# Performance work log

Measured on AMD Instinct MI355X. Metric: run time of the kernel, lower is better.

Reference implementation:

```python
import jax, jax.numpy as jnp
import numpy as np

B = 512          # graphs
M = 200          # nodes per graph
N = B * M        # 102400 total nodes
E = N * 32       # 3,276,800 edges
DIM_IN = 128
K = 30           # SortPool k
F = 32 + 32 + 32 + 1  # concat feature dim = 97


def setup_inputs() -> dict:
    key = jax.random.key(0)
    ks = jax.random.split(key, 20)
    x = jax.random.normal(ks[0], (N, DIM_IN), jnp.float32)
    # within-graph random edges so that batched SortPool is meaningful
    eg = jnp.repeat(jnp.arange(B, dtype=jnp.int32), E // B)  # graph id per edge
    src = eg * M + jax.random.randint(ks[1], (E,), 0, M, dtype=jnp.int32)
    dst = eg * M + jax.random.randint(ks[2], (E,), 0, M, dtype=jnp.int32)
    edge_index = jnp.stack([src, dst])  # [2, E]
    batch = jnp.arange(N, dtype=jnp.int32) // M  # sorted graph assignment

    def lin(k, fi, fo):
        s = 1.0 / np.sqrt(fi)
        return jax.random.uniform(k, (fi, fo), jnp.float32, -s, s)

    inp = {
        "x": x, "edge_index": edge_index, "batch": batch,
        "W1": lin(ks[3], DIM_IN, 32), "b1": jnp.zeros((32,), jnp.float32),
        "W2": lin(ks[4], 32, 32), "b2": jnp.zeros((32,), jnp.float32),
        "W3": lin(ks[5], 32, 32), "b3": jnp.zeros((32,), jnp.float32),
        "W4": lin(ks[6], 32, 1),  "b4": jnp.zeros((1,), jnp.float32),
        "convW1": jax.random.normal(ks[7], (16, 1, 97), jnp.float32) * 0.05,
        "convb1": jnp.zeros((16,), jnp.float32),
        "convW2": jax.random.normal(ks[8], (32, 16, 5), jnp.float32) * 0.05,
        "convb2": jnp.zeros((32,), jnp.float32),
        "linW1": lin(ks[9], 352, 128), "linb1": jnp.zeros((128,), jnp.float32),
        "linW2": lin(ks[10], 128, 1),  "linb2": jnp.zeros((1,), jnp.float32),
    }
    return inp


def _gcn(x, W, b, src, dst, dinv):
    """PyG GCNConv: D^-1/2 (A+I) D^-1/2 X W + b (degrees include self-loops)."""
    xw = x @ W                                   # [N, Fout]
    norm = dinv[src] * dinv[dst]                 # [E]
    agg = jax.ops.segment_sum(xw[src] * norm[:, None], dst, num_segments=N)
    agg = agg + xw * (dinv * dinv)[:, None]      # self-loop term
    return agg + b


def reference(x, edge_index, batch, W1, b1, W2, b2, W3, b3, W4, b4,
              convW1, convb1, convW2, convb2, linW1, linb1, linW2, linb2):
    src, dst = edge_index[0], edge_index[1]
    deg = jax.ops.segment_sum(jnp.ones((E,), x.dtype), dst, num_segments=N) + 1.0
    dinv = jax.lax.rsqrt(deg)

    h1 = jnp.tanh(_gcn(x, W1, b1, src, dst, dinv))
    h2 = jnp.tanh(_gcn(h1, W2, b2, src, dst, dinv))
    h3 = jnp.tanh(_gcn(h2, W3, b3, src, dst, dinv))
    h4 = jnp.tanh(_gcn(h3, W4, b4, src, dst, dinv))
    h = jnp.concatenate([h1, h2, h3, h4], axis=-1)  # [N, 97]

    # SortPool: batch is block-contiguous with M nodes/graph -> dense [B, M, F]
    hd = h.reshape(B, M, F)
    order = jnp.argsort(-hd[:, :, -1], axis=1)[:, :K]          # top-K by last channel
    top = jnp.take_along_axis(hd, order[:, :, None], axis=1)   # [B, K, 97]

    seq = top.reshape(B, 1, K * F)                             # [B, 1, 2910]
    dn = ("NCH", "OIH", "NCH")
    c1 = jax.lax.conv_general_dilated(seq, convW1, (97,), "VALID",
                                      dimension_numbers=dn) + convb1[None, :, None]
    c1 = jax.nn.relu(c1)                                       # [B, 16, 30]
    c1 = c1.reshape(B, 16, 15, 2).max(axis=-1)                 # MaxPool1d(2,2)
    c2 = jax.lax.conv_general_dilated(c1, convW2, (1,), "VALID",
                                      dimension_numbers=dn) + convb2[None, :, None]
    c2 = jax.nn.relu(c2)                                       # [B, 32, 11]

    flat = c2.reshape(B, 352)
    hlin = jax.nn.relu(flat @ linW1 + linb1)                   # dropout = identity (eval)
    out = jax.nn.sigmoid(hlin @ linW2 + linb2)                 # [B, 1]
    return out
```

## Files before the change

### kernel.cpp

```cpp
#include <hip/hip_runtime.h>
#include <hip/hip_fp16.h>


#define TPB   1024
#define GRID  512
#define MG    200
#define EPG   6400
#define EE    (512 * EPG)

#define OFF_BUFX 0
#define OFF_HCUR 28944
#define OFF_CSR  57744
#define OFF_ROFF 64944
#define OFF_CNT  65760
#define OFF_CUR  66560
#define OFF_DINV 67360
#define OFF_H4   68160
#define OFF_RANK 68960
#define OFF_ORD  69760
#define OFF_BIAS 69880
#define OFF_RED  70072
#define OFF_WREG 70144
#define SMEM_BYTES 78336

__global__ __launch_bounds__(TPB)
void dgcnn_kernel(
    const float* __restrict__ x,
    const int*   __restrict__ ei,
    const float* __restrict__ W1, const float* __restrict__ b1,
    const float* __restrict__ W2, const float* __restrict__ b2,
    const float* __restrict__ W3, const float* __restrict__ b3,
    const float* __restrict__ W4, const float* __restrict__ b4,
    const float* __restrict__ cW1, const float* __restrict__ cb1,
    const float* __restrict__ cW2, const float* __restrict__ cb2,
    const float* __restrict__ lW1, const float* __restrict__ lb1,
    const float* __restrict__ lW2, const float* __restrict__ lb2,
    __half* __restrict__ arch,
    float* __restrict__ out)
{
    extern __shared__ unsigned char smem[];
    float* bufX = (float*)(smem + OFF_BUFX);
    float* hcur = (float*)(smem + OFF_HCUR);
    unsigned char* csr = (unsigned char*)(smem + OFF_CSR);
    int*   roff = (int*)(smem + OFF_ROFF);
    int*   cnt  = (int*)(smem + OFF_CNT);
    int*   cur  = (int*)(smem + OFF_CUR);
    float* dinv = (float*)(smem + OFF_DINV);
    float* h4k  = (float*)(smem + OFF_H4);
    int*   rank = (int*)(smem + OFF_RANK);
    int*   ord  = (int*)(smem + OFF_ORD);
    float* bias = (float*)(smem + OFF_BIAS);
    float* red  = (float*)(smem + OFF_RED);
    float* wreg = (float*)(smem + OFF_WREG);

    const int g = blockIdx.x;
    const int t = threadIdx.x;
    const int gbase = g * MG;
    const float* xg   = x + (size_t)gbase * 128;
    const int*   srcp = ei + (size_t)g * EPG;
    const int*   dstp = ei + (size_t)EE + (size_t)g * EPG;

    for (int idx = t; idx < 2048; idx += TPB) wreg[idx] = W1[idx];
    if (t < 32) bias[t] = b1[t];
    if (t < MG) { cnt[t] = 0; rank[t] = 0; }
    if (t >= 512 && t < 548) bufX[200 * 36 + (t - 512)] = 0.f;
    __syncthreads();

    for (int e = t; e < EPG; e += TPB) atomicAdd(&cnt[dstp[e] - gbase], 1);
    __syncthreads();

    if (t >= 256 && t < 256 + MG) {
        int i = t - 256;
        dinv[i] = 1.0f / sqrtf((float)(cnt[i] + 1));
    }
    if (t < 64) {
        if (t == 0) roff[0] = 0;
        int carry = 0;
        #pragma unroll
        for (int c = 0; c < 4; ++c) {
            const int i = c * 64 + t;
            int v = (i < MG) ? ((cnt[i] + 4) & ~3) : 0;
            #pragma unroll
            for (int off = 1; off < 64; off <<= 1) {
                int u = __shfl_up(v, off);
                if (t >= (int)off) v += u;
            }
            if (i < MG) roff[i + 1] = carry + v;
            carry += __shfl(v, 63);
        }
    }
    __syncthreads();

    if (t < MG) {
        int p = roff[t];
        csr[p] = (unsigned char)t;
        cur[t] = p + 1;
    }
    __syncthreads();

    for (int e = t; e < EPG; e += TPB) {
        int d = dstp[e] - gbase;
        int s = srcp[e] - gbase;
        int p = atomicAdd(&cur[d], 1);
        csr[p] = (unsigned char)s;
    }
    __syncthreads();

    if (t < MG) {
        for (int p = cur[t]; p < roff[t + 1]; ++p) csr[p] = (unsigned char)200;
    }
    __syncthreads();

    const int f32lane = t & 31;
    const int islot   = t >> 5;

    auto agg_layer = [&](int archOff) {
        const int fq  = t & 7;
        const int f4  = fq << 2;
        const int dsl = t >> 3;
        for (int d = dsl; d < MG; d += 128) {
            const int p0 = roff[d], p1 = roff[d + 1];
            float a0 = 0.f, a1 = 0.f, a2 = 0.f, a3 = 0.f;
            for (int p = p0; p < p1; p += 4) {
                const unsigned q = *(const unsigned*)(csr + p);
                const float4 v0 = *(const float4*)(bufX + (q & 255u) * 36 + f4);
                const float4 v1 = *(const float4*)(bufX + ((q >> 8) & 255u) * 36 + f4);
                a0 += v0.x; a1 += v0.y; a2 += v0.z; a3 += v0.w;
                a0 += v1.x; a1 += v1.y; a2 += v1.z; a3 += v1.w;
                const float4 v2 = *(const float4*)(bufX + ((q >> 16) & 255u) * 36 + f4);
                const float4 v3 = *(const float4*)(bufX + (q >> 24) * 36 + f4);
                a0 += v2.x; a1 += v2.y; a2 += v2.z; a3 += v2.w;
                a0 += v3.x; a1 += v3.y; a2 += v3.z; a3 += v3.w;
            }
            const float dv = dinv[d];
            const float o0 = tanhf(dv * a0 + bias[f4 + 0]);
            const float o1 = tanhf(dv * a1 + bias[f4 + 1]);
            const float o2 = tanhf(dv * a2 + bias[f4 + 2]);
            const float o3 = tanhf(dv * a3 + bias[f4 + 3]);
            *(float4*)(hcur + d * 36 + f4) = make_float4(o0, o1, o2, o3);
            if (archOff >= 0) {
                const __half2 p01 = __floats2half2_rn(o0, o1);
                const __half2 p23 = __floats2half2_rn(o2, o3);
                __half2* dst = (__half2*)(arch + (size_t)(gbase + d) * 64 + archOff + f4);
                dst[0] = p01;
                dst[1] = p23;
            }
        }
    };

    auto gemm_mid = [&](const float* __restrict__ src) {
        const int f = f32lane;
        {
            float acc0 = 0.f, acc1 = 0.f, acc2 = 0.f, acc3 = 0.f;
            #pragma unroll 2
            for (int k4 = 0; k4 < 8; ++k4) {
                const float w0 = wreg[k4 * 128 + 0  + f];
                const float w1 = wreg[k4 * 128 + 32 + f];
                const float w2 = wreg[k4 * 128 + 64 + f];
                const float w3 = wreg[k4 * 128 + 96 + f];
                float4 v;
                v = *(const float4*)(src + (islot      ) * 36 + k4 * 4); acc0 += v.x*w0 + v.y*w1 + v.z*w2 + v.w*w3;
                v = *(const float4*)(src + (islot + 32 ) * 36 + k4 * 4); acc1 += v.x*w0 + v.y*w1 + v.z*w2 + v.w*w3;
                v = *(const float4*)(src + (islot + 64 ) * 36 + k4 * 4); acc2 += v.x*w0 + v.y*w1 + v.z*w2 + v.w*w3;
                v = *(const float4*)(src + (islot + 96 ) * 36 + k4 * 4); acc3 += v.x*w0 + v.y*w1 + v.z*w2 + v.w*w3;
            }
            bufX[(islot      ) * 36 + f] = dinv[islot      ] * acc0;
            bufX[(islot + 32 ) * 36 + f] = dinv[islot + 32 ] * acc1;
            bufX[(islot + 64 ) * 36 + f] = dinv[islot + 64 ] * acc2;
            bufX[(islot + 96 ) * 36 + f] = dinv[islot + 96 ] * acc3;
        }
        {
            const int i2  = islot + 192;
            const int i2c = i2 < MG ? i2 : (MG - 1);
            float acc0 = 0.f, acc1 = 0.f, acc2 = 0.f;
            #pragma unroll 2
            for (int k4 = 0; k4 < 8; ++k4) {
                const float w0 = wreg[k4 * 128 + 0  + f];
                const float w1 = wreg[k4 * 128 + 32 + f];
                const float w2 = wreg[k4 * 128 + 64 + f];
                const float w3 = wreg[k4 * 128 + 96 + f];
                float4 v;
                v = *(const float4*)(src + (islot + 128) * 36 + k4 * 4); acc0 += v.x*w0 + v.y*w1 + v.z*w2 + v.w*w3;
                v = *(const float4*)(src + (islot + 160) * 36 + k4 * 4); acc1 += v.x*w0 + v.y*w1 + v.z*w2 + v.w*w3;
                v = *(const float4*)(src + (i2c        ) * 36 + k4 * 4); acc2 += v.x*w0 + v.y*w1 + v.z*w2 + v.w*w3;
            }
            bufX[(islot + 128) * 36 + f] = dinv[islot + 128] * acc0;
            bufX[(islot + 160) * 36 + f] = dinv[islot + 160] * acc1;
            if (i2 < MG) bufX[i2 * 36 + f] = dinv[i2] * acc2;
        }
    };

    {
        const int f = f32lane;
        const float4* xv = (const float4*)xg;
        float a0 = 0.f, a1 = 0.f, a2 = 0.f, a3 = 0.f;
        #pragma unroll 2
        for (int k4 = 0; k4 < 16; ++k4) {
            const float w0 = wreg[k4 * 128 + 0  + f];
            const float w1 = wreg[k4 * 128 + 32 + f];
            const float w2 = wreg[k4 * 128 + 64 + f];
            const float w3 = wreg[k4 * 128 + 96 + f];
            float4 v;
            v = xv[(islot      ) * 32 + k4]; a0 += v.x*w0 + v.y*w1 + v.z*w2 + v.w*w3;
            v = xv[(islot + 32 ) * 32 + k4]; a1 += v.x*w0 + v.y*w1 + v.z*w2 + v.w*w3;
            v = xv[(islot + 64 ) * 32 + k4]; a2 += v.x*w0 + v.y*w1 + v.z*w2 + v.w*w3;
            v = xv[(islot + 96 ) * 32 + k4]; a3 += v.x*w0 + v.y*w1 + v.z*w2 + v.w*w3;
        }
        __syncthreads();
        for (int idx = t; idx < 2048; idx += TPB) wreg[idx] = W1[2048 + idx];
        __syncthreads();
        #pragma unroll 2
        for (int k4 = 0; k4 < 16; ++k4) {
            const float w0 = wreg[k4 * 128 + 0  + f];
            const float w1 = wreg[k4 * 128 + 32 + f];
            const float w2 = wreg[k4 * 128 + 64 + f];
            const float w3 = wreg[k4 * 128 + 96 + f];
            float4 v;
            v = xv[(islot      ) * 32 + 16 + k4]; a0 += v.x*w0 + v.y*w1 + v.z*w2 + v.w*w3;
            v = xv[(islot + 32 ) * 32 + 16 + k4]; a1 += v.x*w0 + v.y*w1 + v.z*w2 + v.w*w3;
            v = xv[(islot + 64 ) * 32 + 16 + k4]; a2 += v.x*w0 + v.y*w1 + v.z*w2 + v.w*w3;
            v = xv[(islot + 96 ) * 32 + 16 + k4]; a3 += v.x*w0 + v.y*w1 + v.z*w2 + v.w*w3;
        }
        bufX[(islot      ) * 36 + f] = dinv[islot      ] * a0;
        bufX[(islot + 32 ) * 36 + f] = dinv[islot + 32 ] * a1;
        bufX[(islot + 64 ) * 36 + f] = dinv[islot + 64 ] * a2;
        bufX[(islot + 96 ) * 36 + f] = dinv[islot + 96 ] * a3;
        const int r6  = islot + 192;
        const int r6c = (r6 < MG) ? r6 : (MG - 1);
        float b0v = 0.f, b1v = 0.f, b2v = 0.f;
        #pragma unroll 2
        for (int k4 = 0; k4 < 16; ++k4) {
            const float w0 = wreg[k4 * 128 + 0  + f];
            const float w1 = wreg[k4 * 128 + 32 + f];
            const float w2 = wreg[k4 * 128 + 64 + f];
            const float w3 = wreg[k4 * 128 + 96 + f];
            float4 v;
            v = xv[(islot + 128) * 32 + 16 + k4]; b0v += v.x*w0 + v.y*w1 + v.z*w2 + v.w*w3;
            v = xv[(islot + 160) * 32 + 16 + k4]; b1v += v.x*w0 + v.y*w1 + v.z*w2 + v.w*w3;
            v = xv[(r6c        ) * 32 + 16 + k4]; b2v += v.x*w0 + v.y*w1 + v.z*w2 + v.w*w3;
        }
        __syncthreads();
        for (int idx = t; idx < 2048; idx += TPB) wreg[idx] = W1[idx];
        __syncthreads();
        #pragma unroll 2
        for (int k4 = 0; k4 < 16; ++k4) {
            const float w0 = wreg[k4 * 128 + 0  + f];
            const float w1 = wreg[k4 * 128 + 32 + f];
            const float w2 = wreg[k4 * 128 + 64 + f];
            const float w3 = wreg[k4 * 128 + 96 + f];
            float4 v;
            v = xv[(islot + 128) * 32 + k4]; b0v += v.x*w0 + v.y*w1 + v.z*w2 + v.w*w3;
            v = xv[(islot + 160) * 32 + k4]; b1v += v.x*w0 + v.y*w1 + v.z*w2 + v.w*w3;
            v = xv[(r6c        ) * 32 + k4]; b2v += v.x*w0 + v.y*w1 + v.z*w2 + v.w*w3;
        }
        bufX[(islot + 128) * 36 + f] = dinv[islot + 128] * b0v;
        bufX[(islot + 160) * 36 + f] = dinv[islot + 160] * b1v;
        if (r6 < MG) bufX[r6 * 36 + f] = dinv[r6] * b2v;
    }
    __syncthreads();
    agg_layer(0);
    __syncthreads();

    for (int idx = t; idx < 1024; idx += TPB) wreg[idx] = W2[idx];
    if (t < 32) bias[t] = b2[t];
    __syncthreads();
    gemm_mid(hcur);
    __syncthreads();
    agg_layer(32);
    __syncthreads();

    for (int idx = t; idx < 1024; idx += TPB) wreg[idx] = W3[idx];
    if (t < 32) bias[t] = b3[t];
    __syncthreads();
    gemm_mid(hcur);
    __syncthreads();
    agg_layer(-1);
    __syncthreads();

    float* scl = (float*)(smem + OFF_CNT);
    if (t < MG) {
        float a = 0.f;
        #pragma unroll 8
        for (int k = 0; k < 32; ++k) a += hcur[t * 36 + k] * W4[k];
        scl[t] = dinv[t] * a;
    }
    if (t == 512) scl[200] = 0.f;
    __syncthreads();
    if (t < MG) {
        const int p0 = roff[t], p1 = roff[t + 1];
        float s = 0.f;
        for (int p = p0; p < p1; p += 4) {
            const unsigned q = *(const unsigned*)(csr + p);
            s += scl[q & 255u] + scl[(q >> 8) & 255u]
               + scl[(q >> 16) & 255u] + scl[q >> 24];
        }
        h4k[t] = tanhf(dinv[t] * s + b4[0]);
    }
    __syncthreads();

    if (t < 512) {
        const int i = t & 255;
        const int half = t >> 8;
        if (i < MG) {
            const float vi = h4k[i];
            int r = 0;
            const int j0 = half * 100, j1 = half * 100 + 100;
            for (int j = j0; j < j1; ++j) {
                const float vj = h4k[j];
                r += (vj > vi || (vj == vi && j < i)) ? 1 : 0;
            }
            atomicAdd(&rank[i], r);
        }
    }
    __syncthreads();
    if (t < MG) {
        const int r = rank[t];
        if (r < 30) ord[r] = t;
    }
    __syncthreads();

    float* topv = bufX;
    float* cw   = bufX + 3104;
    for (int idx = t; idx < 1552; idx += TPB) cw[idx] = cW1[idx];
    for (int idx = t; idx < 2560; idx += TPB) cw[1552 + idx] = cW2[idx];
    if (t < 16) bias[t] = cb1[t];
    else if (t < 48) bias[t] = cb2[t - 16];
    for (int idx = t; idx < 2910; idx += TPB) {
        const int kk = idx / 97;
        const int ff = idx - kk * 97;
        const int nd = ord[kk];
        float v;
        if      (ff < 64) v = __half2float(arch[(size_t)(gbase + nd) * 64 + ff]);
        else if (ff < 96) v = hcur[nd * 36 + (ff - 64)];
        else              v = h4k[nd];
        topv[kk * 100 + ff] = v;
    }
    __syncthreads();

    float* c1p2 = hcur;
    float* c1pl = hcur + 480;
    float* flat = hcur + 736;
    float* hlin = hcur + 1088;

    if (t < 480) {
        const int o  = t & 15;
        const int tt = t >> 4;
        float a = bias[o];
        const float* wrow = cw + o * 97;
        const float* trow = topv + tt * 100;
        #pragma unroll 4
        for (int f = 0; f < 97; ++f) a += wrow[f] * trow[f];
        c1p2[o * 30 + tt] = fmaxf(a, 0.f);
    }
    __syncthreads();

    if (t < 240) {
        const int o  = t & 15;
        const int tp = t >> 4;
        c1pl[o * 16 + tp] = fmaxf(c1p2[o * 30 + 2 * tp], c1p2[o * 30 + 2 * tp + 1]);
    }
    __syncthreads();

    if (t < 352) {
        const int o  = t & 31;
        const int tt = t >> 5;
        float a = bias[16 + o];
        const float* w2r = cw + 1552 + o * 80;
        #pragma unroll
        for (int i2 = 0; i2 < 16; ++i2) {
            #pragma unroll
            for (int kk = 0; kk < 5; ++kk)
                a += w2r[i2 * 5 + kk] * c1pl[i2 * 16 + tt + kk];
        }
        flat[o * 11 + tt] = fmaxf(a, 0.f);
    } else if (t >= 512 && t < 640) {
        hlin[t - 512] = lb1[t - 512];
    }
    __syncthreads();

    {
        const int f  = t & 127;
        const int kc = t >> 7;
        float a = 0.f;
        const int k0 = kc * 44;
        #pragma unroll 4
        for (int kk = k0; kk < k0 + 44; ++kk) a += flat[kk] * lW1[kk * 128 + f];
        atomicAdd(&hlin[f], a);
    }
    __syncthreads();

    if (t < 128) {
        float p = fmaxf(hlin[t], 0.f) * lW2[t];
        #pragma unroll
        for (int off = 32; off > 0; off >>= 1) p += __shfl_down(p, off);
        if ((t & 63) == 0) red[t >> 6] = p;
    }
    __syncthreads();
    if (t == 0) {
        const float z = red[0] + red[1] + lb2[0];
        out[g] = 1.f / (1.f + expf(-z));
    }
}

extern "C" void kernel_launch(void* const* d_in, const int* in_sizes, int n_in,
                              void* d_out, int out_size, void* d_ws, size_t ws_size,
                              hipStream_t stream) {
    (void)in_sizes; (void)n_in; (void)out_size; (void)ws_size;
    const float* x   = (const float*)d_in[0];
    const int*   ei  = (const int*)d_in[1];
    const float* W1  = (const float*)d_in[3];  const float* b1  = (const float*)d_in[4];
    const float* W2  = (const float*)d_in[5];  const float* b2  = (const float*)d_in[6];
    const float* W3  = (const float*)d_in[7];  const float* b3  = (const float*)d_in[8];
    const float* W4  = (const float*)d_in[9];  const float* b4  = (const float*)d_in[10];
    const float* cW1 = (const float*)d_in[11]; const float* cb1 = (const float*)d_in[12];
    const float* cW2 = (const float*)d_in[13]; const float* cb2 = (const float*)d_in[14];
    const float* lW1 = (const float*)d_in[15]; const float* lb1 = (const float*)d_in[16];
    const float* lW2 = (const float*)d_in[17]; const float* lb2 = (const float*)d_in[18];
    float* out = (float*)d_out;
    __half* arch = (__half*)d_ws;

    hipFuncSetAttribute((const void*)dgcnn_kernel,
                        hipFuncAttributeMaxDynamicSharedMemorySize, SMEM_BYTES);

    dgcnn_kernel<<<GRID, TPB, SMEM_BYTES, stream>>>(
        x, ei, W1, b1, W2, b2, W3, b3, W4, b4,
        cW1, cb1, cW2, cb2, lW1, lb1, lW2, lb2, arch, out);
}
```

Measured before the change: 281.4 us.

## Halve block size to 512 threads and read W1 directly from global memory

Block size drops from 1024 to 512 threads, and every per-thread loop (aggregation, GEMMs, final linear layer) is rewritten so each thread covers twice as many rows or columns. The first-layer GEMM no longer stages W1 through shared memory in two halves with extra barriers. It reads W1 straight from global memory or cache, which shrinks LDS use and lets more blocks fit per CU. In exchange each block has less parallelism, and the W1 reads are repeated global loads instead of LDS hits.

```diff
diff --git a/kernel.cpp b/kernel.cpp
--- a/kernel.cpp
+++ b/kernel.cpp
@@ -2,7 +2,7 @@
 #include <hip/hip_fp16.h>
 
 
-#define TPB   1024
+#define TPB   512
 #define GRID  512
 #define MG    200
 #define EPG   6400
@@ -21,7 +21,7 @@
 #define OFF_BIAS 69880
 #define OFF_RED  70072
 #define OFF_WREG 70144
-#define SMEM_BYTES 78336
+#define SMEM_BYTES 74240
 
 __global__ __launch_bounds__(TPB)
 void dgcnn_kernel(
@@ -60,10 +60,9 @@
     const int*   srcp = ei + (size_t)g * EPG;
     const int*   dstp = ei + (size_t)EE + (size_t)g * EPG;
 
-    for (int idx = t; idx < 2048; idx += TPB) wreg[idx] = W1[idx];
     if (t < 32) bias[t] = b1[t];
     if (t < MG) { cnt[t] = 0; rank[t] = 0; }
-    if (t >= 512 && t < 548) bufX[200 * 36 + (t - 512)] = 0.f;
+    if (t >= 256 && t < 292) bufX[200 * 36 + (t - 256)] = 0.f;
     __syncthreads();
 
     for (int e = t; e < EPG; e += TPB) atomicAdd(&cnt[dstp[e] - gbase], 1);
@@ -118,7 +117,7 @@
         const int fq  = t & 7;
         const int f4  = fq << 2;
         const int dsl = t >> 3;
-        for (int d = dsl; d < MG; d += 128) {
+        for (int d = dsl; d < MG; d += 64) {
             const int p0 = roff[d], p1 = roff[d + 1];
             float a0 = 0.f, a1 = 0.f, a2 = 0.f, a3 = 0.f;
             for (int p = p0; p < p1; p += 4) {
@@ -150,8 +149,10 @@
 
     auto gemm_mid = [&](const float* __restrict__ src) {
         const int f = f32lane;
-        {
-            float acc0 = 0.f, acc1 = 0.f, acc2 = 0.f, acc3 = 0.f;
+        #pragma unroll
+        for (int j0 = 0; j0 < 12; j0 += 4) {
+            const int r0 = islot + 16 * j0;
+            float a0 = 0.f, a1 = 0.f, a2 = 0.f, a3 = 0.f;
             #pragma unroll 2
             for (int k4 = 0; k4 < 8; ++k4) {
                 const float w0 = wreg[k4 * 128 + 0  + f];
@@ -159,103 +160,70 @@
                 const float w2 = wreg[k4 * 128 + 64 + f];
                 const float w3 = wreg[k4 * 128 + 96 + f];
                 float4 v;
-                v = *(const float4*)(src + (islot      ) * 36 + k4 * 4); acc0 += v.x*w0 + v.y*w1 + v.z*w2 + v.w*w3;
-                v = *(const float4*)(src + (islot + 32 ) * 36 + k4 * 4); acc1 += v.x*w0 + v.y*w1 + v.z*w2 + v.w*w3;
-                v = *(const float4*)(src + (islot + 64 ) * 36 + k4 * 4); acc2 += v.x*w0 + v.y*w1 + v.z*w2 + v.w*w3;
-                v = *(const float4*)(src + (islot + 96 ) * 36 + k4 * 4); acc3 += v.x*w0 + v.y*w1 + v.z*w2 + v.w*w3;
-            }
-            bufX[(islot      ) * 36 + f] = dinv[islot      ] * acc0;
-            bufX[(islot + 32 ) * 36 + f] = dinv[islot + 32 ] * acc1;
-            bufX[(islot + 64 ) * 36 + f] = dinv[islot + 64 ] * acc2;
-            bufX[(islot + 96 ) * 36 + f] = dinv[islot + 96 ] * acc3;
-        }
-        {
-            const int i2  = islot + 192;
-            const int i2c = i2 < MG ? i2 : (MG - 1);
-            float acc0 = 0.f, acc1 = 0.f, acc2 = 0.f;
+                v = *(const float4*)(src + (r0      ) * 36 + k4 * 4); a0 += v.x*w0 + v.y*w1 + v.z*w2 + v.w*w3;
+                v = *(const float4*)(src + (r0 + 16 ) * 36 + k4 * 4); a1 += v.x*w0 + v.y*w1 + v.z*w2 + v.w*w3;
+                v = *(const float4*)(src + (r0 + 32 ) * 36 + k4 * 4); a2 += v.x*w0 + v.y*w1 + v.z*w2 + v.w*w3;
+                v = *(const float4*)(src + (r0 + 48 ) * 36 + k4 * 4); a3 += v.x*w0 + v.y*w1 + v.z*w2 + v.w*w3;
+            }
+            bufX[(r0      ) * 36 + f] = dinv[r0      ] * a0;
+            bufX[(r0 + 16 ) * 36 + f] = dinv[r0 + 16 ] * a1;
+            bufX[(r0 + 32 ) * 36 + f] = dinv[r0 + 32 ] * a2;
+            bufX[(r0 + 48 ) * 36 + f] = dinv[r0 + 48 ] * a3;
+        }
+        if (islot < 8) {
+            const int r = 192 + islot;
+            float a0 = 0.f;
             #pragma unroll 2
             for (int k4 = 0; k4 < 8; ++k4) {
                 const float w0 = wreg[k4 * 128 + 0  + f];
                 const float w1 = wreg[k4 * 128 + 32 + f];
                 const float w2 = wreg[k4 * 128 + 64 + f];
                 const float w3 = wreg[k4 * 128 + 96 + f];
-                float4 v;
-                v = *(const float4*)(src + (islot + 128) * 36 + k4 * 4); acc0 += v.x*w0 + v.y*w1 + v.z*w2 + v.w*w3;
-                v = *(const float4*)(src + (islot + 160) * 36 + k4 * 4); acc1 += v.x*w0 + v.y*w1 + v.z*w2 + v.w*w3;
-                v = *(const float4*)(src + (i2c        ) * 36 + k4 * 4); acc2 += v.x*w0 + v.y*w1 + v.z*w2 + v.w*w3;
-            }
-            bufX[(islot + 128) * 36 + f] = dinv[islot + 128] * acc0;
-            bufX[(islot + 160) * 36 + f] = dinv[islot + 160] * acc1;
-            if (i2 < MG) bufX[i2 * 36 + f] = dinv[i2] * acc2;
+                const float4 v = *(const float4*)(src + r * 36 + k4 * 4);
+                a0 += v.x*w0 + v.y*w1 + v.z*w2 + v.w*w3;
+            }
+            bufX[r * 36 + f] = dinv[r] * a0;
         }
     };
 
     {
         const int f = f32lane;
         const float4* xv = (const float4*)xg;
-        float a0 = 0.f, a1 = 0.f, a2 = 0.f, a3 = 0.f;
-        #pragma unroll 2
-        for (int k4 = 0; k4 < 16; ++k4) {
-            const float w0 = wreg[k4 * 128 + 0  + f];
-            const float w1 = wreg[k4 * 128 + 32 + f];
-            const float w2 = wreg[k4 * 128 + 64 + f];
-            const float w3 = wreg[k4 * 128 + 96 + f];
-            float4 v;
-            v = xv[(islot      ) * 32 + k4]; a0 += v.x*w0 + v.y*w1 + v.z*w2 + v.w*w3;
-            v = xv[(islot + 32 ) * 32 + k4]; a1 += v.x*w0 + v.y*w1 + v.z*w2 + v.w*w3;
-            v = xv[(islot + 64 ) * 32 + k4]; a2 += v.x*w0 + v.y*w1 + v.z*w2 + v.w*w3;
-            v = xv[(islot + 96 ) * 32 + k4]; a3 += v.x*w0 + v.y*w1 + v.z*w2 + v.w*w3;
-        }
-        __syncthreads();
-        for (int idx = t; idx < 2048; idx += TPB) wreg[idx] = W1[2048 + idx];
-        __syncthreads();
-        #pragma unroll 2
-        for (int k4 = 0; k4 < 16; ++k4) {
-            const float w0 = wreg[k4 * 128 + 0  + f];
-            const float w1 = wreg[k4 * 128 + 32 + f];
-            const float w2 = wreg[k4 * 128 + 64 + f];
-            const float w3 = wreg[k4 * 128 + 96 + f];
-            float4 v;
-            v = xv[(islot      ) * 32 + 16 + k4]; a0 += v.x*w0 + v.y*w1 + v.z*w2 + v.w*w3;
-            v = xv[(islot + 32 ) * 32 + 16 + k4]; a1 += v.x*w0 + v.y*w1 + v.z*w2 + v.w*w3;
-            v = xv[(islot + 64 ) * 32 + 16 + k4]; a2 += v.x*w0 + v.y*w1 + v.z*w2 + v.w*w3;
-            v = xv[(islot + 96 ) * 32 + 16 + k4]; a3 += v.x*w0 + v.y*w1 + v.z*w2 + v.w*w3;
-        }
-        bufX[(islot      ) * 36 + f] = dinv[islot      ] * a0;
-        bufX[(islot + 32 ) * 36 + f] = dinv[islot + 32 ] * a1;
-        bufX[(islot + 64 ) * 36 + f] = dinv[islot + 64 ] * a2;
-        bufX[(islot + 96 ) * 36 + f] = dinv[islot + 96 ] * a3;
-        const int r6  = islot + 192;
-        const int r6c = (r6 < MG) ? r6 : (MG - 1);
-        float b0v = 0.f, b1v = 0.f, b2v = 0.f;
-        #pragma unroll 2
-        for (int k4 = 0; k4 < 16; ++k4) {
-            const float w0 = wreg[k4 * 128 + 0  + f];
-            const float w1 = wreg[k4 * 128 + 32 + f];
-            const float w2 = wreg[k4 * 128 + 64 + f];
-            const float w3 = wreg[k4 * 128 + 96 + f];
-            float4 v;
-            v = xv[(islot + 128) * 32 + 16 + k4]; b0v += v.x*w0 + v.y*w1 + v.z*w2 + v.w*w3;
-            v = xv[(islot + 160) * 32 + 16 + k4]; b1v += v.x*w0 + v.y*w1 + v.z*w2 + v.w*w3;
-            v = xv[(r6c        ) * 32 + 16 + k4]; b2v += v.x*w0 + v.y*w1 + v.z*w2 + v.w*w3;
-        }
-        __syncthreads();
-        for (int idx = t; idx < 2048; idx += TPB) wreg[idx] = W1[idx];
-        __syncthreads();
-        #pragma unroll 2
-        for (int k4 = 0; k4 < 16; ++k4) {
-            const float w0 = wreg[k4 * 128 + 0  + f];
-            const float w1 = wreg[k4 * 128 + 32 + f];
-            const float w2 = wreg[k4 * 128 + 64 + f];
-            const float w3 = wreg[k4 * 128 + 96 + f];
-            float4 v;
-            v = xv[(islot + 128) * 32 + k4]; b0v += v.x*w0 + v.y*w1 + v.z*w2 + v.w*w3;
-            v = xv[(islot + 160) * 32 + k4]; b1v += v.x*w0 + v.y*w1 + v.z*w2 + v.w*w3;
-            v = xv[(r6c        ) * 32 + k4]; b2v += v.x*w0 + v.y*w1 + v.z*w2 + v.w*w3;
-        }
-        bufX[(islot + 128) * 36 + f] = dinv[islot + 128] * b0v;
-        bufX[(islot + 160) * 36 + f] = dinv[islot + 160] * b1v;
-        if (r6 < MG) bufX[r6 * 36 + f] = dinv[r6] * b2v;
+        #pragma unroll
+        for (int j0 = 0; j0 < 12; j0 += 4) {
+            const int r0 = islot + 16 * j0;
+            float a0 = 0.f, a1 = 0.f, a2 = 0.f, a3 = 0.f;
+            #pragma unroll 2
+            for (int k4 = 0; k4 < 32; ++k4) {
+                const float w0 = W1[k4 * 128 + 0  + f];
+                const float w1 = W1[k4 * 128 + 32 + f];
+                const float w2 = W1[k4 * 128 + 64 + f];
+                const float w3 = W1[k4 * 128 + 96 + f];
+                float4 v;
+                v = xv[(r0      ) * 32 + k4]; a0 += v.x*w0 + v.y*w1 + v.z*w2 + v.w*w3;
+                v = xv[(r0 + 16 ) * 32 + k4]; a1 += v.x*w0 + v.y*w1 + v.z*w2 + v.w*w3;
+                v = xv[(r0 + 32 ) * 32 + k4]; a2 += v.x*w0 + v.y*w1 + v.z*w2 + v.w*w3;
+                v = xv[(r0 + 48 ) * 32 + k4]; a3 += v.x*w0 + v.y*w1 + v.z*w2 + v.w*w3;
+            }
+            bufX[(r0      ) * 36 + f] = dinv[r0      ] * a0;
+            bufX[(r0 + 16 ) * 36 + f] = dinv[r0 + 16 ] * a1;
+            bufX[(r0 + 32 ) * 36 + f] = dinv[r0 + 32 ] * a2;
+            bufX[(r0 + 48 ) * 36 + f] = dinv[r0 + 48 ] * a3;
+        }
+        if (islot < 8) {
+            const int r = 192 + islot;
+            float a0 = 0.f;
+            #pragma unroll 2
+            for (int k4 = 0; k4 < 32; ++k4) {
+                const float w0 = W1[k4 * 128 + 0  + f];
+                const float w1 = W1[k4 * 128 + 32 + f];
+                const float w2 = W1[k4 * 128 + 64 + f];
+                const float w3 = W1[k4 * 128 + 96 + f];
+                const float4 v = xv[r * 32 + k4];
+                a0 += v.x*w0 + v.y*w1 + v.z*w2 + v.w*w3;
+            }
+            bufX[r * 36 + f] = dinv[r] * a0;
+        }
     }
     __syncthreads();
     agg_layer(0);
@@ -284,7 +252,7 @@
         for (int k = 0; k < 32; ++k) a += hcur[t * 36 + k] * W4[k];
         scl[t] = dinv[t] * a;
     }
-    if (t == 512) scl[200] = 0.f;
+    if (t == 200) scl[200] = 0.f;
     __syncthreads();
     if (t < MG) {
         const int p0 = roff[t], p1 = roff[t + 1];
@@ -298,7 +266,7 @@
     }
     __syncthreads();
 
-    if (t < 512) {
+    {
         const int i = t & 255;
         const int half = t >> 8;
         if (i < MG) {
@@ -373,8 +341,8 @@
                 a += w2r[i2 * 5 + kk] * c1pl[i2 * 16 + tt + kk];
         }
         flat[o * 11 + tt] = fmaxf(a, 0.f);
-    } else if (t >= 512 && t < 640) {
-        hlin[t - 512] = lb1[t - 512];
+    } else if (t >= 352 && t < 480) {
+        hlin[t - 352] = lb1[t - 352];
     }
     __syncthreads();
 
@@ -382,9 +350,9 @@
         const int f  = t & 127;
         const int kc = t >> 7;
         float a = 0.f;
-        const int k0 = kc * 44;
+        const int k0 = kc * 88;
         #pragma unroll 4
-        for (int kk = k0; kk < k0 + 44; ++kk) a += flat[kk] * lW1[kk * 128 + f];
+        for (int kk = k0; kk < k0 + 88; ++kk) a += flat[kk] * lW1[kk * 128 + f];
         atomicAdd(&hlin[f], a);
     }
     __syncthreads();
```

Result: faster. 268.1 us (-4.7%).
